# Performance work log

Hardware: AMD Instinct MI355X
Metric: run time of the kernel (lower is better)

## Reference

```python
import jax, jax.numpy as jnp
import numpy as np

B, C, H, W = 4, 128, 96, 96
E = 4
C8 = C // 8


def _conv1x1(w, b, x):
    # w: [out, in], x: [b, in, H, W]
    return jnp.einsum('oi,bihw->bohw', w, x) + b[None, :, None, None]


def _bilinear_zeros(x, gx, gy):
    # x: [b, C, h, w]; gx, gy: [b, H2, W2] normalized coords in [-1, 1]
    # align_corners=True, padding_mode='zeros' (matches F.grid_sample)
    b, c, h, w = x.shape
    ix = (gx + 1.0) * 0.5 * (w - 1)
    iy = (gy + 1.0) * 0.5 * (h - 1)
    ix0 = jnp.floor(ix)
    iy0 = jnp.floor(iy)
    tx = ix - ix0
    ty = iy - iy0
    ix0 = ix0.astype(jnp.int32)
    iy0 = iy0.astype(jnp.int32)

    def gather(yy, xx):
        valid = ((xx >= 0) & (xx < w) & (yy >= 0) & (yy < h)).astype(x.dtype)
        xc = jnp.clip(xx, 0, w - 1)
        yc = jnp.clip(yy, 0, h - 1)
        vals = jax.vmap(lambda xb, y, xi: xb[:, y, xi])(x, yc, xc)  # [b,C,H2,W2]
        return vals * valid[:, None]

    w00 = ((1 - tx) * (1 - ty))[:, None]
    w01 = (tx * (1 - ty))[:, None]
    w10 = ((1 - tx) * ty)[:, None]
    w11 = (tx * ty)[:, None]
    return (gather(iy0, ix0) * w00 + gather(iy0, ix0 + 1) * w01
            + gather(iy0 + 1, ix0) * w10 + gather(iy0 + 1, ix0 + 1) * w11)


def setup_inputs() -> dict:
    key = jax.random.key(0)
    ks = jax.random.split(key, 12)
    s = 0.05
    return {
        'x': jax.random.normal(ks[0], (B, C, H, W), jnp.float32),
        'weight_compress': jax.random.normal(ks[1], (E, C8, C), jnp.float32) * s,
        'weight_expand': jax.random.normal(ks[2], (E, C, C8), jnp.float32) * s,
        'body_w1': jax.random.normal(ks[3], (64, 3), jnp.float32) * s,
        'body_b1': jax.random.normal(ks[4], (64,), jnp.float32) * s,
        'body_w2': jax.random.normal(ks[5], (64, 64), jnp.float32) * s,
        'body_b2': jax.random.normal(ks[6], (64,), jnp.float32) * s,
        'rout_w': jax.random.normal(ks[7], (E, 64), jnp.float32) * s,
        'rout_b': jax.random.normal(ks[8], (E,), jnp.float32) * s,
        'off_w': jax.random.normal(ks[9], (2, 64), jnp.float32) * s,
        'off_b': jax.random.normal(ks[10], (2,), jnp.float32) * s,
        'scale': 2,
    }


def reference(x, weight_compress, weight_expand, body_w1, body_b1,
              body_w2, body_b2, rout_w, rout_b, off_w, off_b, scale):
    b, c, h, w = x.shape
    sc = float(scale)
    H2 = round(h * sc)
    W2 = round(w * sc)

    # fractional sub-pixel coordinates (meta-upsample positional encoding)
    ch = (jnp.arange(H2, dtype=jnp.float32) + 0.5) / sc
    ch = ch - jnp.floor(ch + 0.001) - 0.5  # [H2]
    cw = (jnp.arange(W2, dtype=jnp.float32) + 0.5) / sc
    cw = cw - jnp.floor(cw + 0.001) - 0.5  # [W2]
    inp = jnp.stack([
        jnp.full((H2, W2), 1.0 / sc, jnp.float32),
        jnp.broadcast_to(ch[:, None], (H2, W2)),
        jnp.broadcast_to(cw[None, :], (H2, W2)),
    ], axis=0)[None]  # [1, 3, H2, W2]

    emb = jax.nn.relu(_conv1x1(body_w1, body_b1, inp))
    emb = jax.nn.relu(_conv1x1(body_w2, body_b2, emb))
    offset = _conv1x1(off_w, off_b, emb)                      # [1, 2, H2, W2]
    routing = jax.nn.sigmoid(_conv1x1(rout_w, rout_b, emb))   # [1, E, H2, W2]
    r = routing[0].transpose(1, 2, 0)                         # [H2, W2, E]

    # base sampling grid, align_corners=True normalization + learned offset
    gx = ((jnp.arange(W2, dtype=jnp.float32) + 0.5) / sc - 0.5) * 2.0 / (w - 1) - 1.0
    gy = ((jnp.arange(H2, dtype=jnp.float32) + 0.5) / sc - 0.5) * 2.0 / (h - 1) - 1.0
    gx = gx[None, None, :] + offset[:, 0] * 2.0 / (w - 1)     # [1, H2, W2]
    gy = gy[None, :, None] + offset[:, 1] * 2.0 / (h - 1)
    gx = jnp.broadcast_to(gx, (b, H2, W2))
    gy = jnp.broadcast_to(gy, (b, H2, W2))

    fea0 = _bilinear_zeros(x, gx, gy)          # [b, C, H2, W2]
    fea = fea0.transpose(0, 2, 3, 1)           # [b, H2, W2, C]

    # per-pixel routed 1x1 convs: compress (C->C/8) then expand (C/8->C)
    comp = jnp.einsum('bhwc,hwe,eoc->bhwo', fea, r, weight_compress)
    out = jnp.einsum('bhwo,hwe,eco->bhwc', comp, r, weight_expand)
    return out.transpose(0, 3, 1, 2) + fea0
```

## Files before the change

### kernel.cpp

```cpp
#include <hip/hip_runtime.h>
#include <math.h>

#define Bn 4
#define Cc 128
#define Hh 96
#define Ww 96
#define H2c 192
#define W2c 192
#define HW (Hh*Ww)

#define WC_OFF 0
#define WE_OFF (4*2048)
#define TAP_OFF (8*2048)
#define M_OFF  16640

typedef float  f32x4  __attribute__((ext_vector_type(4)));
typedef short  s16x8  __attribute__((ext_vector_type(8)));

__device__ __forceinline__ unsigned f2bf(float f) {
    unsigned u = __float_as_uint(f);
    return (u + 0x7FFFu + ((u >> 16) & 1u)) >> 16;
}

__global__ __launch_bounds__(256) void k1_mix(
    const float* __restrict__ wcomp, const float* __restrict__ wexp,
    const float* __restrict__ bw1, const float* __restrict__ bb1,
    const float* __restrict__ bw2, const float* __restrict__ bb2,
    const float* __restrict__ rw,  const float* __restrict__ rb,
    const float* __restrict__ ow,  const float* __restrict__ ob,
    float* __restrict__ ws)
{
    __shared__ float e1[64], e2[64], rr[4], of[2];
    const int tid   = threadIdx.x;
    const int cls   = blockIdx.x >> 4;
    const int chunk = blockIdx.x & 15;
    const float chv = (cls & 2) ? 0.25f : -0.25f;
    const float cwv = (cls & 1) ? 0.25f : -0.25f;

    if (tid < 64) {
        float h = bw1[tid*3+0]*0.5f + bw1[tid*3+1]*chv + bw1[tid*3+2]*cwv + bb1[tid];
        e1[tid] = fmaxf(h, 0.f);
    }
    __syncthreads();
    if (tid < 64) {
        float s = bb2[tid];
        for (int i = 0; i < 64; ++i) s += bw2[tid*64+i]*e1[i];
        e2[tid] = fmaxf(s, 0.f);
    }
    __syncthreads();
    if (tid < 6) {
        if (tid < 4) {
            float s = rb[tid];
            for (int i = 0; i < 64; ++i) s += rw[tid*64+i]*e2[i];
            rr[tid] = 1.f/(1.f+expf(-s));
        } else {
            const int d = tid - 4;
            float s = ob[d];
            for (int i = 0; i < 64; ++i) s += ow[d*64+i]*e2[i];
            of[d] = s;
        }
    }
    __syncthreads();
    const float r0 = rr[0], r1 = rr[1], r2 = rr[2], r3 = rr[3];

    if (tid < 128) {
        const int idx = chunk*128 + tid;
        const int o = idx >> 7, c = idx & 127;
        const float v = r0*wcomp[idx] + r1*wcomp[2048+idx]
                      + r2*wcomp[4096+idx] + r3*wcomp[6144+idx];
        ws[WC_OFF + cls*2048 + c*16 + o] = v;
    } else {
        const int idx = chunk*128 + (tid - 128);
        ws[WE_OFF + cls*2048 + idx] =
            r0*wexp[idx] + r1*wexp[2048+idx] + r2*wexp[4096+idx] + r3*wexp[6144+idx];
    }
    if (chunk == 0 && tid == 0) {
        const float fx = cwv + of[0];
        const float fy = chv + of[1];
        const float Dx = floorf(fx), Dy = floorf(fy);
        ws[TAP_OFF + cls*4 + 0] = fx - Dx;
        ws[TAP_OFF + cls*4 + 1] = fy - Dy;
        ws[TAP_OFF + cls*4 + 2] = Dx;
        ws[TAP_OFF + cls*4 + 3] = Dy;
    }
}

__global__ __launch_bounds__(256) void k1b_fold(
    const float* __restrict__ wsr, unsigned short* __restrict__ Mw)
{
    const int t   = blockIdx.x*256 + threadIdx.x;
    const int cls = t >> 12;
    const int rem = t & 4095;
    const int co  = rem >> 5;
    const int ci0 = (rem & 31) * 4;
    const float* we = wsr + WE_OFF + cls*2048 + co*16;

    float m[4];
    #pragma unroll
    for (int q = 0; q < 4; ++q) {
        const float* wc = wsr + WC_OFF + cls*2048 + (ci0+q)*16;
        float s = 0.f;
        #pragma unroll
        for (int o = 0; o < 16; ++o) s += we[o]*wc[o];
        if (co == ci0 + q) s += 1.f;
        m[q] = s;
    }
    uint2 v;
    v.x = f2bf(m[0]) | (f2bf(m[1]) << 16);
    v.y = f2bf(m[2]) | (f2bf(m[3]) << 16);
    *reinterpret_cast<uint2*>(Mw + (size_t)cls*16384 + co*128 + ci0) = v;
}

__device__ __forceinline__ void remap_axis(int c0, int last, float w0, float w1,
                                           int& base, float& a0, float& a1)
{
    base = min(max(c0, 0), last - 1);
    if (c0 >= 0 && c0 < last) { a0 = w0;  a1 = w1;  }
    else if (c0 == -1)        { a0 = w1;  a1 = 0.f; }
    else if (c0 == last)      { a0 = 0.f; a1 = w0;  }
    else                      { a0 = 0.f; a1 = 0.f; }
}

__global__ __launch_bounds__(256) void k2_mfma(
    const float* __restrict__ x, const float* __restrict__ wsr,
    const unsigned short* __restrict__ Mw, float* __restrict__ out)
{
    __shared__ __align__(16) unsigned short lF[64*128];

    const int tid = threadIdx.x;
    const int xl  = tid & 63;
    const int grp = tid >> 6;

    const int n = blockIdx.x;
    const int w = (n & 7) * 288 + (n >> 3);
    const int px_ = w & 1, py = (w >> 1) & 1;
    const int w2 = w >> 2;
    const int tile = w2 % 144;
    const int b    = w2 / 144;
    const int cls  = (py << 1) | px_;

    const int pix = tile*64 + xl;
    const int j = pix / 96;
    const int i = pix - j*96;

    const float tx = wsr[TAP_OFF + cls*4 + 0];
    const float ty = wsr[TAP_OFF + cls*4 + 1];
    const int   Dx = (int)wsr[TAP_OFF + cls*4 + 2];
    const int   Dy = (int)wsr[TAP_OFF + cls*4 + 3];
    int cb, rbw; float ax0, ax1, ay0, ay1;
    remap_axis(i + Dx, Ww - 1, 1.f - tx, tx, cb,  ax0, ax1);
    remap_axis(j + Dy, Hh - 1, 1.f - ty, ty, rbw, ay0, ay1);
    const float w00 = ay0*ax0, w01 = ay0*ax1, w10 = ay1*ax0, w11 = ay1*ax1;
    const float* xb = x + (size_t)b*Cc*HW + rbw*Ww + cb;

    #pragma unroll
    for (int q = 0; q < 8; ++q) {
        const int c = grp*32 + q*4;
        const float* p0 = xb + (size_t)(c  )*HW;
        const float* p1 = xb + (size_t)(c+1)*HW;
        const float* p2 = xb + (size_t)(c+2)*HW;
        const float* p3 = xb + (size_t)(c+3)*HW;
        const float f0 = w00*p0[0] + w01*p0[1] + w10*p0[Ww] + w11*p0[Ww+1];
        const float f1 = w00*p1[0] + w01*p1[1] + w10*p1[Ww] + w11*p1[Ww+1];
        const float f2 = w00*p2[0] + w01*p2[1] + w10*p2[Ww] + w11*p2[Ww+1];
        const float f3 = w00*p3[0] + w01*p3[1] + w10*p3[Ww] + w11*p3[Ww+1];
        uint2 v;
        v.x = f2bf(f0) | (f2bf(f1) << 16);
        v.y = f2bf(f2) | (f2bf(f3) << 16);
        int byte = xl*256 + c*2;
        byte ^= (xl & 7) << 4;
        *reinterpret_cast<uint2*>(reinterpret_cast<char*>(lF) + byte) = v;
    }

    const unsigned short* Mc = Mw + (size_t)cls*16384;
    s16x8 a[2][4];
    #pragma unroll
    for (int t = 0; t < 2; ++t)
        #pragma unroll
        for (int kk = 0; kk < 4; ++kk) {
            const int row = 32*grp + 16*t + (xl & 15);
            const unsigned short* ap = Mc + row*128 + kk*32 + ((xl >> 4) & 3)*8;
            a[t][kk] = *reinterpret_cast<const s16x8*>(ap);
        }

    __syncthreads();

    f32x4 acc[2][4];
    #pragma unroll
    for (int t = 0; t < 2; ++t)
        #pragma unroll
        for (int nn = 0; nn < 4; ++nn) acc[t][nn] = (f32x4){0.f, 0.f, 0.f, 0.f};

    #pragma unroll
    for (int kk = 0; kk < 4; ++kk) {
        #pragma unroll
        for (int nn = 0; nn < 4; ++nn) {
            int byte = (nn*16 + (xl & 15))*256 + kk*64 + ((xl >> 4) & 3)*16;
            byte ^= (xl & 7) << 4;
            const s16x8 bf = *reinterpret_cast<const s16x8*>(
                reinterpret_cast<const char*>(lF) + byte);
            acc[0][nn] = __builtin_amdgcn_mfma_f32_16x16x32_bf16(a[0][kk], bf, acc[0][nn], 0, 0, 0);
            acc[1][nn] = __builtin_amdgcn_mfma_f32_16x16x32_bf16(a[1][kk], bf, acc[1][nn], 0, 0, 0);
        }
    }

    #pragma unroll
    for (int t = 0; t < 2; ++t)
        #pragma unroll
        for (int nn = 0; nn < 4; ++nn) {
            const int pix2 = tile*64 + nn*16 + (xl & 15);
            const int j2 = pix2 / 96;
            const int i2 = pix2 - j2*96;
            const int yg = 2*j2 + py;
            const int xg = 2*i2 + px_;
            const int ch0 = 32*grp + 16*t + ((xl >> 4) & 3)*4;
            float* op = out + ((size_t)(b*Cc + ch0)*H2c + yg)*W2c + xg;
            #pragma unroll
            for (int r = 0; r < 4; ++r)
                op[(size_t)r*(H2c*W2c)] = acc[t][nn][r];
        }
}

extern "C" void kernel_launch(void* const* d_in, const int* in_sizes, int n_in,
                              void* d_out, int out_size, void* d_ws, size_t ws_size,
                              hipStream_t stream) {
    const float* x     = (const float*)d_in[0];
    const float* wcomp = (const float*)d_in[1];
    const float* wexp  = (const float*)d_in[2];
    const float* bw1   = (const float*)d_in[3];
    const float* bb1   = (const float*)d_in[4];
    const float* bw2   = (const float*)d_in[5];
    const float* bb2   = (const float*)d_in[6];
    const float* rw    = (const float*)d_in[7];
    const float* rb    = (const float*)d_in[8];
    const float* ow    = (const float*)d_in[9];
    const float* ob    = (const float*)d_in[10];
    float* out = (float*)d_out;
    float* ws  = (float*)d_ws;
    unsigned short* Mw = (unsigned short*)(ws + M_OFF);

    k1_mix<<<64, 256, 0, stream>>>(wcomp, wexp, bw1, bb1, bw2, bb2, rw, rb, ow, ob, ws);
    k1b_fold<<<64, 256, 0, stream>>>(ws, Mw);
    k2_mfma<<<2304, 256, 0, stream>>>(x, ws, Mw, out);
}
```

Baseline: 49.23 us.

## Retile upsample GEMM by output row segments for contiguous vectorized stores

```diff
diff --git a/kernel.cpp b/kernel.cpp
--- a/kernel.cpp
+++ b/kernel.cpp
@@ -121,27 +121,28 @@
     else                      { a0 = 0.f; a1 = 0.f; }
 }
 
-__global__ __launch_bounds__(256) void k2_mfma(
+__global__ __launch_bounds__(256, 4) void k2_mfma(
     const float* __restrict__ x, const float* __restrict__ wsr,
     const unsigned short* __restrict__ Mw, float* __restrict__ out)
 {
     __shared__ __align__(16) unsigned short lF[64*128];
 
     const int tid = threadIdx.x;
-    const int xl  = tid & 63;
+    const int l   = tid & 63;
     const int grp = tid >> 6;
 
-    const int n = blockIdx.x;
-    const int w = (n & 7) * 288 + (n >> 3);
-    const int px_ = w & 1, py = (w >> 1) & 1;
-    const int w2 = w >> 2;
-    const int tile = w2 % 144;
-    const int b    = w2 / 144;
-    const int cls  = (py << 1) | px_;
-
-    const int pix = tile*64 + xl;
-    const int j = pix / 96;
-    const int i = pix - j*96;
+    const int n  = blockIdx.x;
+    const int g  = (n & 7)*288 + (n >> 3);
+    const int b  = g / 576;
+    const int r  = g % 576;
+    const int yg = r / 3;
+    const int xt = r % 3;
+
+    const int s   = l;
+    const int par = s >> 5;
+    const int i   = xt*32 + (s & 31);
+    const int j   = yg >> 1;
+    const int cls = ((yg & 1) << 1) | par;
 
     const float tx = wsr[TAP_OFF + cls*4 + 0];
     const float ty = wsr[TAP_OFF + cls*4 + 1];
@@ -152,73 +153,98 @@
     remap_axis(j + Dy, Hh - 1, 1.f - ty, ty, rbw, ay0, ay1);
     const float w00 = ay0*ax0, w01 = ay0*ax1, w10 = ay1*ax0, w11 = ay1*ax1;
     const float* xb = x + (size_t)b*Cc*HW + rbw*Ww + cb;
-
-    #pragma unroll
-    for (int q = 0; q < 8; ++q) {
-        const int c = grp*32 + q*4;
-        const float* p0 = xb + (size_t)(c  )*HW;
-        const float* p1 = xb + (size_t)(c+1)*HW;
-        const float* p2 = xb + (size_t)(c+2)*HW;
-        const float* p3 = xb + (size_t)(c+3)*HW;
-        const float f0 = w00*p0[0] + w01*p0[1] + w10*p0[Ww] + w11*p0[Ww+1];
-        const float f1 = w00*p1[0] + w01*p1[1] + w10*p1[Ww] + w11*p1[Ww+1];
-        const float f2 = w00*p2[0] + w01*p2[1] + w10*p2[Ww] + w11*p2[Ww+1];
-        const float f3 = w00*p3[0] + w01*p3[1] + w10*p3[Ww] + w11*p3[Ww+1];
-        uint2 v;
-        v.x = f2bf(f0) | (f2bf(f1) << 16);
-        v.y = f2bf(f2) | (f2bf(f3) << 16);
-        int byte = xl*256 + c*2;
-        byte ^= (xl & 7) << 4;
-        *reinterpret_cast<uint2*>(reinterpret_cast<char*>(lF) + byte) = v;
-    }
-
-    const unsigned short* Mc = Mw + (size_t)cls*16384;
-    s16x8 a[2][4];
+    const int chbase = grp*32;
+
+#define LOADB(t0,t1,t2,t3,base) \
+    _Pragma("unroll") \
+    for (int k = 0; k < 8; ++k) { \
+        const float* p = xb + (size_t)(chbase + (base) + k)*HW; \
+        t0[k] = p[0]; t1[k] = p[1]; t2[k] = p[Ww]; t3[k] = p[Ww+1]; \
+    }
+
+#define CONSB(t0,t1,t2,t3,base) \
+    _Pragma("unroll") \
+    for (int k = 0; k < 8; k += 4) { \
+        const float f0 = w00*t0[k  ] + w01*t1[k  ] + w10*t2[k  ] + w11*t3[k  ]; \
+        const float f1 = w00*t0[k+1] + w01*t1[k+1] + w10*t2[k+1] + w11*t3[k+1]; \
+        const float f2 = w00*t0[k+2] + w01*t1[k+2] + w10*t2[k+2] + w11*t3[k+2]; \
+        const float f3 = w00*t0[k+3] + w01*t1[k+3] + w10*t2[k+3] + w11*t3[k+3]; \
+        uint2 v; \
+        v.x = f2bf(f0) | (f2bf(f1) << 16); \
+        v.y = f2bf(f2) | (f2bf(f3) << 16); \
+        const int c = chbase + (base) + k; \
+        int byte = l*256 + c*2; \
+        byte ^= (l & 7) << 4; \
+        *reinterpret_cast<uint2*>(reinterpret_cast<char*>(lF) + byte) = v; \
+    }
+
+    {
+        float a0[8], a1[8], a2[8], a3[8];
+        float b0[8], b1[8], b2[8], b3[8];
+        LOADB(a0,a1,a2,a3, 0)
+        LOADB(b0,b1,b2,b3, 8)
+        __builtin_amdgcn_sched_barrier(0);
+        CONSB(a0,a1,a2,a3, 0)
+        LOADB(a0,a1,a2,a3, 16)
+        __builtin_amdgcn_sched_barrier(0);
+        CONSB(b0,b1,b2,b3, 8)
+        LOADB(b0,b1,b2,b3, 24)
+        __builtin_amdgcn_sched_barrier(0);
+        CONSB(a0,a1,a2,a3, 16)
+        __builtin_amdgcn_sched_barrier(0);
+        CONSB(b0,b1,b2,b3, 24)
+    }
+    __syncthreads();
+
+    f32x4 acc[2][4];
     #pragma unroll
     for (int t = 0; t < 2; ++t)
         #pragma unroll
+        for (int nn = 0; nn < 4; ++nn) acc[t][nn] = (f32x4){0.f, 0.f, 0.f, 0.f};
+
+    const int lo = l & 15, hi = l >> 4;
+    #pragma unroll
+    for (int ph = 0; ph < 2; ++ph) {
+        const unsigned short* Mc = Mw + (size_t)(((yg & 1) << 1) | ph)*16384;
+        s16x8 mf[2][4];
+        #pragma unroll
+        for (int t = 0; t < 2; ++t)
+            #pragma unroll
+            for (int kk = 0; kk < 4; ++kk)
+                mf[t][kk] = *reinterpret_cast<const s16x8*>(
+                    Mc + (32*grp + 16*t + lo)*128 + kk*32 + hi*8);
+        #pragma unroll
         for (int kk = 0; kk < 4; ++kk) {
-            const int row = 32*grp + 16*t + (xl & 15);
-            const unsigned short* ap = Mc + row*128 + kk*32 + ((xl >> 4) & 3)*8;
-            a[t][kk] = *reinterpret_cast<const s16x8*>(ap);
+            #pragma unroll
+            for (int q = 0; q < 2; ++q) {
+                const int nn = ph*2 + q;
+                const int row = nn*16 + lo;
+                int byte = row*256 + kk*64 + hi*16;
+                byte ^= (row & 7) << 4;
+                const s16x8 af = *reinterpret_cast<const s16x8*>(
+                    reinterpret_cast<const char*>(lF) + byte);
+                acc[0][nn] = __builtin_amdgcn_mfma_f32_16x16x32_bf16(af, mf[0][kk], acc[0][nn], 0, 0, 0);
+                acc[1][nn] = __builtin_amdgcn_mfma_f32_16x16x32_bf16(af, mf[1][kk], acc[1][nn], 0, 0, 0);
+            }
         }
-
-    __syncthreads();
-
-    f32x4 acc[2][4];
-    #pragma unroll
-    for (int t = 0; t < 2; ++t)
-        #pragma unroll
-        for (int nn = 0; nn < 4; ++nn) acc[t][nn] = (f32x4){0.f, 0.f, 0.f, 0.f};
-
-    #pragma unroll
-    for (int kk = 0; kk < 4; ++kk) {
-        #pragma unroll
-        for (int nn = 0; nn < 4; ++nn) {
-            int byte = (nn*16 + (xl & 15))*256 + kk*64 + ((xl >> 4) & 3)*16;
-            byte ^= (xl & 7) << 4;
-            const s16x8 bf = *reinterpret_cast<const s16x8*>(
-                reinterpret_cast<const char*>(lF) + byte);
-            acc[0][nn] = __builtin_amdgcn_mfma_f32_16x16x32_bf16(a[0][kk], bf, acc[0][nn], 0, 0, 0);
-            acc[1][nn] = __builtin_amdgcn_mfma_f32_16x16x32_bf16(a[1][kk], bf, acc[1][nn], 0, 0, 0);
+    }
+
+    #pragma unroll
+    for (int t = 0; t < 2; ++t) {
+        const int ch = 32*grp + 16*t + lo;
+        #pragma unroll
+        for (int p = 0; p < 2; ++p) {
+            const f32x4 e = acc[t][p], o = acc[t][p+2];
+            const f32x4 v0 = {e[0], o[0], e[1], o[1]};
+            const f32x4 v1 = {e[2], o[2], e[3], o[3]};
+            float* op = out + ((size_t)(b*Cc + ch)*H2c + yg)*W2c
+                      + xt*64 + p*32 + hi*8;
+            *reinterpret_cast<f32x4*>(op)     = v0;
+            *reinterpret_cast<f32x4*>(op + 4) = v1;
         }
     }
-
-    #pragma unroll
-    for (int t = 0; t < 2; ++t)
-        #pragma unroll
-        for (int nn = 0; nn < 4; ++nn) {
-            const int pix2 = tile*64 + nn*16 + (xl & 15);
-            const int j2 = pix2 / 96;
-            const int i2 = pix2 - j2*96;
-            const int yg = 2*j2 + py;
-            const int xg = 2*i2 + px_;
-            const int ch0 = 32*grp + 16*t + ((xl >> 4) & 3)*4;
-            float* op = out + ((size_t)(b*Cc + ch0)*H2c + yg)*W2c + xg;
-            #pragma unroll
-            for (int r = 0; r < 4; ++r)
-                op[(size_t)r*(H2c*W2c)] = acc[t][nn][r];
-        }
+#undef LOADB
+#undef CONSB
 }
 
 extern "C" void kernel_launch(void* const* d_in, const int* in_sizes, int n_in,
```

New measurement: 56.99 us. 1.16x slower.
